# Performance work log

Measured on AMD Instinct MI355X. Metric: run time of the kernel, lower is better.

The kernel has to match this reference:

```python
import jax, jax.numpy as jnp
import numpy as np

DOWN = 2
KCONV = 3

def _blur_kernel():
    # _setup_kernel([1,3,3,1]): outer product, normalize; is_ref flips it.
    k = np.array([1.0, 3.0, 3.0, 1.0], dtype=np.float32)
    K = np.outer(k, k)
    K /= K.sum()
    K = K[::-1, ::-1].copy()  # torch.flip(dims=(0,1)) (symmetric here, kept for fidelity)
    return jnp.asarray(K)  # [4,4]

def setup_inputs() -> dict:
    key = jax.random.key(0)
    k1, k2, k3 = jax.random.split(key, 3)
    x = jax.random.normal(k1, (16, 256, 128, 128), dtype=jnp.float32)
    weight = jax.random.normal(k2, (512, 256, KCONV, KCONV), dtype=jnp.float32)  # OIHW
    bias = jax.random.normal(k3, (512,), dtype=jnp.float32)
    return {"x": x, "weight": weight, "bias": bias, "blur_k": _blur_kernel()}

def reference(x, weight, bias, blur_k):
    N, C, H, W = x.shape
    Wb = blur_k.shape[-1]
    # pad sizes: p = Wb - down + (Wconv - 1)
    p = Wb - DOWN + (KCONV - 1)
    pad0, pad1 = (p + 1) // 2, p // 2
    # upfirdn_2d (up=down=1): pad + depthwise FIR correlation with the (pre-flipped) kernel
    kd = jnp.broadcast_to(blur_k[None, None], (C, 1, Wb, Wb))  # depthwise OIHW
    xb = jax.lax.conv_general_dilated(
        x, kd, window_strides=(1, 1),
        padding=[(pad0, pad1), (pad0, pad1)],
        feature_group_count=C,
        dimension_numbers=("NCHW", "OIHW", "NCHW"))  # [N,C,129,129]
    # EqualizedLRConv2d: runtime weight scaling 1/sqrt(fan_in), stride=2, no padding
    fan_in = weight.shape[1] * weight.shape[2] * weight.shape[3]
    scale = 1.0 / np.sqrt(fan_in)
    y = jax.lax.conv_general_dilated(
        xb, weight * jnp.float32(scale), window_strides=(DOWN, DOWN),
        padding="VALID",
        dimension_numbers=("NCHW", "OIHW", "NCHW"))  # [N,512,64,64]
    return y + bias[None, :, None, None]
```

## Files before the change

kernel.cpp:

```cpp
#include <hip/hip_runtime.h>
#include <hip/hip_bf16.h>
#include <stdint.h>
#include <stddef.h>

#define NB   16
#define CIN  256
#define HIN  128
#define WIN  128
#define COUT 512
#define HO   64
#define WO   64
#define HBL  129

typedef __attribute__((ext_vector_type(8))) __bf16 bf16x8;
typedef __attribute__((ext_vector_type(4))) float  f32x4;

__device__ __forceinline__ void gld_lds16(const void* g, void* l) {
  __builtin_amdgcn_global_load_lds(
      (const __attribute__((address_space(1))) void*)g,
      (__attribute__((address_space(3))) void*)l, 16, 0, 0);
}

__device__ __forceinline__ unsigned pack_bf16(float lo, float hi) {
  __hip_bfloat16 l = __float2bfloat16(lo), h = __float2bfloat16(hi);
  unsigned short ul = *(unsigned short*)&l, uh = *(unsigned short*)&h;
  return (unsigned)ul | ((unsigned)uh << 16);
}

__global__ __launch_bounds__(512) void blur_kernel(
    const float* __restrict__ x,
    const float* __restrict__ bk,
    __hip_bfloat16* __restrict__ xb)
{
  __shared__ __hip_bfloat16 lout[CIN * 130];

  const int bid0 = blockIdx.x;
  const int bid  = (bid0 & 7) * 258 + (bid0 >> 3);
  const int n    = bid / HBL;
  const int io   = bid % HBL;
  const int t    = threadIdx.x;
  const int wave = t >> 6;
  const int lane = t & 63;
  const int half = lane >> 5;
  const int g    = lane & 31;

  const float K11 = bk[5];
  float a[4], b[4];
  #pragma unroll
  for (int u = 0; u < 4; ++u) a[u] = bk[u * 4 + 1] / K11;
  #pragma unroll
  for (int v = 0; v < 4; ++v) b[v] = bk[4 + v];

  int rr[4];
  #pragma unroll
  for (int u = 0; u < 4; ++u) {
    int r = io - 2 + u;
    if (r < 0 || r >= HIN) { a[u] = 0.f; r = 0; }
    rr[u] = r;
  }

  #pragma unroll 2
  for (int cb = wave * 2; cb < CIN; cb += 16) {
    const int c = cb + half;
    const float4* xr = (const float4*)(x + ((size_t)(n * CIN + c) * HIN) * WIN);
    float4 vm = {0.f, 0.f, 0.f, 0.f};
    #pragma unroll
    for (int u = 0; u < 4; ++u) {
      const float4 rv = xr[rr[u] * 32 + g];
      vm.x += a[u] * rv.x; vm.y += a[u] * rv.y;
      vm.z += a[u] * rv.z; vm.w += a[u] * rv.w;
    }
    float vmm2 = __shfl_up(vm.z, 1);
    float vmm1 = __shfl_up(vm.w, 1);
    float vmp4 = __shfl_down(vm.x, 1);
    if (g == 0)  { vmm2 = 0.f; vmm1 = 0.f; }
    if (g == 31) { vmp4 = 0.f; }
    const float o0 = b[0]*vmm2 + b[1]*vmm1 + b[2]*vm.x + b[3]*vm.y;
    const float o1 = b[0]*vmm1 + b[1]*vm.x + b[2]*vm.y + b[3]*vm.z;
    const float o2 = b[0]*vm.x + b[1]*vm.y + b[2]*vm.z + b[3]*vm.w;
    const float o3 = b[0]*vm.y + b[1]*vm.z + b[2]*vm.w + b[3]*vmp4;
    unsigned* dst = (unsigned*)&lout[c * 130 + 4 * g];
    dst[0] = pack_bf16(o0, o1);
    dst[1] = pack_bf16(o2, o3);
    if (g == 31)
      lout[c * 130 + 128] = __float2bfloat16(b[0]*vm.z + b[1]*vm.w);
  }

  __syncthreads();

  const size_t obase = ((size_t)(n * HBL + io)) * HBL * CIN;
  for (int e = t; e < 65 * 64; e += 512) {
    const int jp = e >> 6;
    const int l  = e & 63;
    const unsigned r0 = *(const unsigned*)&lout[(4*l + 0) * 130 + 2*jp];
    const unsigned r1 = *(const unsigned*)&lout[(4*l + 1) * 130 + 2*jp];
    const unsigned r2 = *(const unsigned*)&lout[(4*l + 2) * 130 + 2*jp];
    const unsigned r3 = *(const unsigned*)&lout[(4*l + 3) * 130 + 2*jp];
    uint2 s0, s1;
    s0.x = (r0 & 0xffffu) | (r1 << 16);
    s0.y = (r2 & 0xffffu) | (r3 << 16);
    s1.x = (r0 >> 16) | (r1 & 0xffff0000u);
    s1.y = (r2 >> 16) | (r3 & 0xffff0000u);
    *(uint2*)&xb[obase + (size_t)(2*jp) * CIN + 4*l] = s0;
    if (jp < 64)
      *(uint2*)&xb[obase + (size_t)(2*jp + 1) * CIN + 4*l] = s1;
  }
}

__global__ __launch_bounds__(256) void wprep_kernel(
    const float* __restrict__ w,
    __hip_bfloat16* __restrict__ wt)
{
  const int idx = blockIdx.x * 256 + threadIdx.x;
  if (idx >= 9 * COUT * CIN) return;
  const int c   = idx & (CIN - 1);
  const int o   = (idx >> 8) & (COUT - 1);
  const int tap = idx >> 17;
  wt[idx] = __float2bfloat16(w[(o * CIN + c) * 9 + tap]);
}

__global__ __launch_bounds__(512, 2) void gemm_kernel(
    const __hip_bfloat16* __restrict__ xb,
    const __hip_bfloat16* __restrict__ wt,
    const float* __restrict__ bias,
    float* __restrict__ y)
{
  __shared__ __align__(16) char lds[4 * 32768];

  const int t    = threadIdx.x;
  const int wave = t >> 6;
  const int lane = t & 63;
  const int bid0 = blockIdx.x;
  const int bid  = (bid0 & 7) * 64 + (bid0 >> 3);
  const int nb   = bid & 1;
  const int mb   = bid >> 1;
  const int o0   = nb * 256;
  const int p0   = mb * 256;
  const int imgn = p0 >> 12;
  const int h0   = (p0 >> 6) & 63;

  const int wo  = wave >> 2;
  const int wp  = wave & 3;
  const int q   = lane >> 4;
  const int m16 = lane & 15;

  long xg[2], wg[2];
  int  ldsoff[2];
  #pragma unroll
  for (int s = 0; s < 2; ++s) {
    const int ia = wave * 2 + s;
    const int Lr = ia * 8 + (lane >> 3);
    const int g3 = (lane & 7) ^ (Lr & 7);
    const int r  = 2 * Lr + (g3 >> 2);
    const int cq = (g3 & 3) * 8;
    const int hh = h0 + (r >> 6);
    const int ww = r & 63;
    xg[s] = ((long)(imgn * HBL + 2 * hh) * HBL + 2 * ww) * CIN + cq;
    wg[s] = (long)(o0 + r) * CIN + cq;
    ldsoff[s] = ia * 1024;
  }

  int aoff[8];
  #pragma unroll
  for (int of = 0; of < 8; ++of) {
    const int r  = wo * 128 + of * 16 + m16;
    const int g3 = (((r & 1) << 2) | q) ^ ((r >> 1) & 7);
    aoff[of] = (r >> 1) * 128 + g3 * 16;
  }
  int boff[4];
  #pragma unroll
  for (int pf = 0; pf < 4; ++pf) {
    const int r  = wp * 64 + pf * 16 + m16;
    const int g3 = (((r & 1) << 2) | q) ^ ((r >> 1) & 7);
    boff[pf] = (r >> 1) * 128 + g3 * 16;
  }

  f32x4 acc[8][4];
  #pragma unroll
  for (int of = 0; of < 8; ++of)
    #pragma unroll
    for (int pf = 0; pf < 4; ++pf)
      acc[of][pf] = (f32x4){0.f, 0.f, 0.f, 0.f};

  auto stage = [&](int kt) {
    const int  slot = kt & 3;
    const int  tap  = kt >> 3;
    const int  cb   = (kt & 7) * 32;
    const long xoff = (long)((tap / 3) * HBL + (tap % 3)) * CIN + cb;
    const long woff = (long)tap * (COUT * CIN) + cb;
    char* sb = &lds[slot * 32768];
    #pragma unroll
    for (int s = 0; s < 2; ++s) {
      gld_lds16(wt + woff + wg[s], sb + ldsoff[s]);
      gld_lds16(xb + xoff + xg[s], sb + 16384 + ldsoff[s]);
    }
  };

  auto compute = [&](int kt) {
    const char* sb = &lds[(kt & 3) * 32768];
    bf16x8 aw[8], bx[4];
    #pragma unroll
    for (int of = 0; of < 8; ++of)
      aw[of] = *(const bf16x8*)(sb + aoff[of]);
    #pragma unroll
    for (int pf = 0; pf < 4; ++pf)
      bx[pf] = *(const bf16x8*)(sb + 16384 + boff[pf]);
    __builtin_amdgcn_s_setprio(1);
    #pragma unroll
    for (int of = 0; of < 8; ++of)
      #pragma unroll
      for (int pf = 0; pf < 4; ++pf)
        acc[of][pf] = __builtin_amdgcn_mfma_f32_16x16x32_bf16(
            aw[of], bx[pf], acc[of][pf], 0, 0, 0);
    __builtin_amdgcn_s_setprio(0);
  };

  stage(0); stage(1); stage(2);

  for (int kt = 0; kt < 69; ++kt) {
    stage(kt + 3);
    asm volatile("s_waitcnt vmcnt(12)" ::: "memory");
    __builtin_amdgcn_s_barrier();
    __builtin_amdgcn_sched_barrier(0);
    compute(kt);
    __builtin_amdgcn_sched_barrier(0);
    __builtin_amdgcn_s_barrier();
  }
  asm volatile("s_waitcnt vmcnt(8)" ::: "memory");
  __builtin_amdgcn_s_barrier();
  __builtin_amdgcn_sched_barrier(0);
  compute(69);
  __builtin_amdgcn_sched_barrier(0);
  __builtin_amdgcn_s_barrier();
  asm volatile("s_waitcnt vmcnt(4)" ::: "memory");
  __builtin_amdgcn_s_barrier();
  __builtin_amdgcn_sched_barrier(0);
  compute(70);
  __builtin_amdgcn_sched_barrier(0);
  __builtin_amdgcn_s_barrier();
  asm volatile("s_waitcnt vmcnt(0)" ::: "memory");
  __builtin_amdgcn_s_barrier();
  __builtin_amdgcn_sched_barrier(0);
  compute(71);

  const float scale = 1.0f / 48.0f;
  #pragma unroll
  for (int of = 0; of < 8; ++of) {
    const int o = o0 + wo * 128 + of * 16 + q * 4;
    #pragma unroll
    for (int pf = 0; pf < 4; ++pf) {
      const int p  = p0 + wp * 64 + pf * 16 + m16;
      const int n  = p >> 12;
      const int hh = (p >> 6) & 63;
      const int ww = p & 63;
      const size_t obase = ((size_t)(n * COUT + o) * HO + hh) * WO + ww;
      #pragma unroll
      for (int rg = 0; rg < 4; ++rg) {
        const float v = acc[of][pf][rg] * scale + bias[o + rg];
        y[obase + (size_t)rg * (HO * WO)] = v;
      }
    }
  }
}

extern "C" void kernel_launch(void* const* d_in, const int* in_sizes, int n_in,
                              void* d_out, int out_size, void* d_ws, size_t ws_size,
                              hipStream_t stream) {
  const float* x  = (const float*)d_in[0];
  const float* w  = (const float*)d_in[1];
  const float* bs = (const float*)d_in[2];
  const float* bk = (const float*)d_in[3];
  float* y = (float*)d_out;

  __hip_bfloat16* xb = (__hip_bfloat16*)d_ws;
  __hip_bfloat16* wt = (__hip_bfloat16*)((char*)d_ws +
                       (size_t)NB * HBL * HBL * CIN * sizeof(__hip_bfloat16));

  hipLaunchKernelGGL(blur_kernel, dim3(NB * HBL), dim3(512), 0, stream, x, bk, xb);
  hipLaunchKernelGGL(wprep_kernel, dim3((9 * COUT * CIN + 255) / 256), dim3(256), 0, stream, w, wt);
  hipLaunchKernelGGL(gemm_kernel, dim3(256 * 2), dim3(512), 0, stream,
                     xb, wt, bs, y);
}
```

Before: 572.9 us.

## Split each K-step into two half-phases to interleave LDS reads with MFMA

Restructures the main loop into a two-phase ping-pong schedule. Each iteration first loads half of the A fragments plus all B fragments and issues the next global-to-LDS stage, then runs the first 16 MFMAs. It then loads the second half of the A fragments and runs the remaining MFMAs. The goal is to overlap LDS reads and global prefetch with MFMA work across waves and to lower register pressure. The cost is more barriers per iteration, and the vmcnt accounting is rewritten, so it has to exactly match the number of loads in flight.

```diff
diff --git a/kernel.cpp b/kernel.cpp
--- a/kernel.cpp
+++ b/kernel.cpp
@@ -196,52 +196,58 @@
     }
   };
 
-  auto compute = [&](int kt) {
+  stage(0); stage(1); stage(2);
+  asm volatile("s_waitcnt vmcnt(8)" ::: "memory");
+  __builtin_amdgcn_s_barrier();
+
+  for (int kt = 0; kt < 72; ++kt) {
     const char* sb = &lds[(kt & 3) * 32768];
-    bf16x8 aw[8], bx[4];
-    #pragma unroll
-    for (int of = 0; of < 8; ++of)
-      aw[of] = *(const bf16x8*)(sb + aoff[of]);
-    #pragma unroll
-    for (int pf = 0; pf < 4; ++pf)
-      bx[pf] = *(const bf16x8*)(sb + 16384 + boff[pf]);
+    __builtin_amdgcn_sched_barrier(0);
+
+    bf16x8 aw0[4], bx[4];
+    #pragma unroll
+    for (int i = 0; i < 4; ++i)
+      aw0[i] = *(const bf16x8*)(sb + aoff[i]);
+    #pragma unroll
+    for (int i = 0; i < 4; ++i)
+      bx[i] = *(const bf16x8*)(sb + 16384 + boff[i]);
+    if (kt < 69) stage(kt + 3);
+    __builtin_amdgcn_s_barrier();
+    asm volatile("s_waitcnt lgkmcnt(0)" ::: "memory");
+    __builtin_amdgcn_sched_barrier(0);
     __builtin_amdgcn_s_setprio(1);
     #pragma unroll
-    for (int of = 0; of < 8; ++of)
+    for (int of = 0; of < 4; ++of)
       #pragma unroll
       for (int pf = 0; pf < 4; ++pf)
         acc[of][pf] = __builtin_amdgcn_mfma_f32_16x16x32_bf16(
-            aw[of], bx[pf], acc[of][pf], 0, 0, 0);
+            aw0[of], bx[pf], acc[of][pf], 0, 0, 0);
     __builtin_amdgcn_s_setprio(0);
-  };
-
-  stage(0); stage(1); stage(2);
-
-  for (int kt = 0; kt < 69; ++kt) {
-    stage(kt + 3);
-    asm volatile("s_waitcnt vmcnt(12)" ::: "memory");
-    __builtin_amdgcn_s_barrier();
-    __builtin_amdgcn_sched_barrier(0);
-    compute(kt);
-    __builtin_amdgcn_sched_barrier(0);
-    __builtin_amdgcn_s_barrier();
-  }
-  asm volatile("s_waitcnt vmcnt(8)" ::: "memory");
-  __builtin_amdgcn_s_barrier();
-  __builtin_amdgcn_sched_barrier(0);
-  compute(69);
-  __builtin_amdgcn_sched_barrier(0);
-  __builtin_amdgcn_s_barrier();
-  asm volatile("s_waitcnt vmcnt(4)" ::: "memory");
-  __builtin_amdgcn_s_barrier();
-  __builtin_amdgcn_sched_barrier(0);
-  compute(70);
-  __builtin_amdgcn_sched_barrier(0);
-  __builtin_amdgcn_s_barrier();
-  asm volatile("s_waitcnt vmcnt(0)" ::: "memory");
-  __builtin_amdgcn_s_barrier();
-  __builtin_amdgcn_sched_barrier(0);
-  compute(71);
+    __builtin_amdgcn_sched_barrier(0);
+    __builtin_amdgcn_s_barrier();
+    __builtin_amdgcn_sched_barrier(0);
+
+    bf16x8 aw1[4];
+    #pragma unroll
+    for (int i = 0; i < 4; ++i)
+      aw1[i] = *(const bf16x8*)(sb + aoff[4 + i]);
+    if (kt <= 68)      asm volatile("s_waitcnt vmcnt(8)" ::: "memory");
+    else if (kt == 69) asm volatile("s_waitcnt vmcnt(4)" ::: "memory");
+    else               asm volatile("s_waitcnt vmcnt(0)" ::: "memory");
+    __builtin_amdgcn_s_barrier();
+    asm volatile("s_waitcnt lgkmcnt(0)" ::: "memory");
+    __builtin_amdgcn_sched_barrier(0);
+    __builtin_amdgcn_s_setprio(1);
+    #pragma unroll
+    for (int of = 0; of < 4; ++of)
+      #pragma unroll
+      for (int pf = 0; pf < 4; ++pf)
+        acc[4 + of][pf] = __builtin_amdgcn_mfma_f32_16x16x32_bf16(
+            aw1[of], bx[pf], acc[4 + of][pf], 0, 0, 0);
+    __builtin_amdgcn_s_setprio(0);
+    __builtin_amdgcn_sched_barrier(0);
+    __builtin_amdgcn_s_barrier();
+  }
 
   const float scale = 1.0f / 48.0f;
   #pragma unroll
```

Measured after the change: 578.0 us. About the same (+0.9%).

## Double-buffer MFMA register fragments to overlap LDS reads with matrix math

Applied to the files above, without the earlier changes.

Restructures the main loop so the LDS fragments for the next k-step are read into a second register set while MFMAs run on the current set. The two barriers per iteration become one, and the vmcnt waits are rearranged to fit. Fragment offsets are now computed from a single base plus a constant stride instead of per-fragment arrays. This hides LDS read latency behind compute, at the cost of more VGPRs for the duplicate fragment buffers, which could reduce occupancy or cause spills.

```diff
diff --git a/kernel.cpp b/kernel.cpp
--- a/kernel.cpp
+++ b/kernel.cpp
@@ -160,20 +160,9 @@
     ldsoff[s] = ia * 1024;
   }
 
-  int aoff[8];
-  #pragma unroll
-  for (int of = 0; of < 8; ++of) {
-    const int r  = wo * 128 + of * 16 + m16;
-    const int g3 = (((r & 1) << 2) | q) ^ ((r >> 1) & 7);
-    aoff[of] = (r >> 1) * 128 + g3 * 16;
-  }
-  int boff[4];
-  #pragma unroll
-  for (int pf = 0; pf < 4; ++pf) {
-    const int r  = wp * 64 + pf * 16 + m16;
-    const int g3 = (((r & 1) << 2) | q) ^ ((r >> 1) & 7);
-    boff[pf] = (r >> 1) * 128 + g3 * 16;
-  }
+  const int g3f   = (((m16 & 1) << 2) | q) ^ ((m16 >> 1) & 7);
+  const int abase = ((wo * 128 + m16) >> 1) * 128 + g3f * 16;
+  const int bbase = ((wp * 64  + m16) >> 1) * 128 + g3f * 16;
 
   f32x4 acc[8][4];
   #pragma unroll
@@ -196,15 +185,16 @@
     }
   };
 
-  auto compute = [&](int kt) {
-    const char* sb = &lds[(kt & 3) * 32768];
-    bf16x8 aw[8], bx[4];
-    #pragma unroll
-    for (int of = 0; of < 8; ++of)
-      aw[of] = *(const bf16x8*)(sb + aoff[of]);
-    #pragma unroll
-    for (int pf = 0; pf < 4; ++pf)
-      bx[pf] = *(const bf16x8*)(sb + 16384 + boff[pf]);
+  auto read_frags = [&](bf16x8 (&aw)[8], bf16x8 (&bx)[4], const char* sb) {
+    #pragma unroll
+    for (int i = 0; i < 8; ++i)
+      aw[i] = *(const bf16x8*)(sb + abase + i * 1024);
+    #pragma unroll
+    for (int i = 0; i < 4; ++i)
+      bx[i] = *(const bf16x8*)(sb + 16384 + bbase + i * 1024);
+  };
+
+  auto mfma_tile = [&](const bf16x8 (&aw)[8], const bf16x8 (&bx)[4]) {
     __builtin_amdgcn_s_setprio(1);
     #pragma unroll
     for (int of = 0; of < 8; ++of)
@@ -215,33 +205,34 @@
     __builtin_amdgcn_s_setprio(0);
   };
 
-  stage(0); stage(1); stage(2);
-
-  for (int kt = 0; kt < 69; ++kt) {
-    stage(kt + 3);
-    asm volatile("s_waitcnt vmcnt(12)" ::: "memory");
+  bf16x8 awA[8], bxA[4], awB[8], bxB[4];
+
+  auto body = [&](int kt, bf16x8 (&cAW)[8], bf16x8 (&cBX)[4],
+                  bf16x8 (&nAW)[8], bf16x8 (&nBX)[4]) {
+    if (kt <= 68) stage(kt + 3);
+    if (kt < 71)
+      read_frags(nAW, nBX, &lds[((kt + 1) & 3) * 32768]);
+    mfma_tile(cAW, cBX);
+    asm volatile("s_waitcnt lgkmcnt(0)" ::: "memory");
+    __builtin_amdgcn_sched_barrier(0);
+    if (kt <= 68)      asm volatile("s_waitcnt vmcnt(4)" ::: "memory");
+    else if (kt == 69) asm volatile("s_waitcnt vmcnt(0)" ::: "memory");
     __builtin_amdgcn_s_barrier();
     __builtin_amdgcn_sched_barrier(0);
-    compute(kt);
-    __builtin_amdgcn_sched_barrier(0);
-    __builtin_amdgcn_s_barrier();
-  }
-  asm volatile("s_waitcnt vmcnt(8)" ::: "memory");
-  __builtin_amdgcn_s_barrier();
-  __builtin_amdgcn_sched_barrier(0);
-  compute(69);
-  __builtin_amdgcn_sched_barrier(0);
-  __builtin_amdgcn_s_barrier();
+  };
+
+  stage(0); stage(1); stage(2);
   asm volatile("s_waitcnt vmcnt(4)" ::: "memory");
   __builtin_amdgcn_s_barrier();
   __builtin_amdgcn_sched_barrier(0);
-  compute(70);
+  read_frags(awA, bxA, &lds[0]);
+  asm volatile("s_waitcnt lgkmcnt(0)" ::: "memory");
   __builtin_amdgcn_sched_barrier(0);
-  __builtin_amdgcn_s_barrier();
-  asm volatile("s_waitcnt vmcnt(0)" ::: "memory");
-  __builtin_amdgcn_s_barrier();
-  __builtin_amdgcn_sched_barrier(0);
-  compute(71);
+
+  for (int ktp = 0; ktp < 72; ktp += 2) {
+    body(ktp,     awA, bxA, awB, bxB);
+    body(ktp + 1, awB, bxB, awA, bxA);
+  }
 
   const float scale = 1.0f / 48.0f;
   #pragma unroll
```

Result: no change. 562.4 us (-1.8%).
